# Optimization experiments

Measured on AMD Instinct MI355X. Metric: run time of the kernel, lower is better.

Reference implementation:

```python
import jax, jax.numpy as jnp
import numpy as np

E = 8        # num_experts
TOPK = 2     # num_experts_per_tok
D = 1024     # n_embd
H = 2816     # grok FFN hidden dim (multiple_of-rounded 2/3*4*D)
B, T = 4, 2048
COEFF = 0.01 # moe_aux_loss_coeff


def setup_inputs() -> dict:
    key = jax.random.key(0)
    ks = jax.random.split(key, 8)
    s = 0.02  # weight scale so activations stay well-conditioned
    return {
        "x": jax.random.normal(ks[0], (B, T, D), jnp.float32),
        "gate_w": jax.random.normal(ks[1], (D, E), jnp.float32) * s,
        "expert_gate": jax.random.normal(ks[2], (E, D, H), jnp.float32) * s,
        "expert_up": jax.random.normal(ks[3], (E, D, H), jnp.float32) * s,
        "expert_down": jax.random.normal(ks[4], (E, H, D), jnp.float32) * s,
        "shared_gate": jax.random.normal(ks[5], (D, H), jnp.float32) * s,
        "shared_up": jax.random.normal(ks[6], (D, H), jnp.float32) * s,
        "shared_down": jax.random.normal(ks[7], (H, D), jnp.float32) * s,
    }


def _grok_ffn(x, g, u, d):
    # down(gelu(gate(x)) * up(x)); torch F.gelu default = exact erf gelu
    return (jax.nn.gelu(x @ g, approximate=False) * (x @ u)) @ d


def reference(x, gate_w, expert_gate, expert_up, expert_down,
              shared_gate, shared_up, shared_down):
    Bb, Tt, Dd = x.shape
    N = Bb * Tt
    xf = x.reshape(N, Dd)

    # --- router ---
    logits = (xf @ gate_w).astype(jnp.float32)            # (N, E)
    top_logits, top_idx = jax.lax.top_k(logits, TOPK)     # (N, K)
    top_w = jax.nn.softmax(top_logits, axis=-1)           # (N, K)
    gates = jax.nn.softmax(logits, axis=-1)               # (N, E)
    f = jnp.mean(jax.nn.one_hot(top_idx[:, 0], E, dtype=jnp.float32), axis=0)
    P = gates.mean(axis=0)
    aux_loss = COEFF * E * jnp.sum(f * P)

    # dense combine weights (N, E): 0 for unassigned experts
    comb = jnp.zeros((N, E), xf.dtype).at[
        jnp.arange(N)[:, None], top_idx].add(top_w.astype(xf.dtype))

    # --- experts: loop over small fixed E, weight-masked dense FFN ---
    out = jnp.zeros_like(xf)
    for e in range(E):
        ye = _grok_ffn(xf, expert_gate[e], expert_up[e], expert_down[e])
        out = out + comb[:, e:e + 1] * ye

    out = out.reshape(Bb, Tt, Dd)
    out = out + _grok_ffn(xf, shared_gate, shared_up, shared_down).reshape(Bb, Tt, Dd)
    return out, aux_loss
```

## Files before the change

### kernel.cpp

```cpp
#include <hip/hip_runtime.h>
#include <hip/hip_bf16.h>

#define NTOK 8192
#define DIM  1024
#define HID  2816
#define ROWS_CAP 25600
#define TCAP 200

typedef __bf16 bf16x8 __attribute__((ext_vector_type(8)));
typedef float  f32x4  __attribute__((ext_vector_type(4)));

__device__ __forceinline__ unsigned short f2bf(float f) {
  unsigned int x = __float_as_uint(f);
  unsigned int r = (x + 0x7fffu + ((x >> 16) & 1u)) >> 16;
  return (unsigned short)r;
}
__device__ __forceinline__ float gelu_erf(float g) {
  return 0.5f * g * (1.0f + erff(g * 0.70710678118654752f));
}

__device__ __forceinline__ void gload16(const void* g, void* l) {
  __builtin_amdgcn_global_load_lds(
      (__attribute__((address_space(1))) void*)(g),
      (__attribute__((address_space(3))) void*)(l), 16, 0, 0);
}


__global__ __launch_bounds__(256) void k_cast_bf16(const float4* __restrict__ in,
                                                   ushort4* __restrict__ out, int n4) {
  int i = blockIdx.x * 256 + threadIdx.x;
  if (i >= n4) return;
  float4 v = in[i];
  out[i] = make_ushort4(f2bf(v.x), f2bf(v.y), f2bf(v.z), f2bf(v.w));
}

__global__ __launch_bounds__(256) void k_transpose_bf16(const float* __restrict__ in,
                                                        unsigned short* __restrict__ out,
                                                        int R, int C) {
  __shared__ float t[32][33];
  size_t base = (size_t)blockIdx.z * R * C;
  in += base; out += base;
  int c0 = blockIdx.x * 32, r0 = blockIdx.y * 32;
  int tx = threadIdx.x, ty = threadIdx.y;
  #pragma unroll
  for (int i = ty; i < 32; i += 8)
    t[i][tx] = in[(size_t)(r0 + i) * C + c0 + tx];
  __syncthreads();
  #pragma unroll
  for (int i = ty; i < 32; i += 8)
    out[(size_t)(c0 + i) * R + r0 + tx] = f2bf(t[tx][i]);
}


__global__ __launch_bounds__(256) void k_router(const float* __restrict__ x,
                                                const float* __restrict__ gw,
                                                int* __restrict__ top_idx,
                                                float* __restrict__ top_w,
                                                int* __restrict__ counts,
                                                float* __restrict__ f_cnt,
                                                float* __restrict__ P_sum) {
  __shared__ float s_p[8];
  __shared__ int   s_cnt[8];
  __shared__ int   s_f[8];
  int tid = threadIdx.x;
  if (tid < 8) { s_p[tid] = 0.f; s_cnt[tid] = 0; s_f[tid] = 0; }
  __syncthreads();

  int lane = tid & 63, wv = tid >> 6;
  float ploc[8] = {0,0,0,0,0,0,0,0};
  int   cloc[8] = {0,0,0,0,0,0,0,0};
  int   floc[8] = {0,0,0,0,0,0,0,0};

  for (int t = blockIdx.x * 4 + wv; t < NTOK; t += 1024) {
    const float* xr = x + (size_t)t * DIM;
    float acc[8] = {0.f,0.f,0.f,0.f,0.f,0.f,0.f,0.f};
    for (int d = lane; d < DIM; d += 64) {
      float xv = xr[d];
      const float* g = gw + d * 8;
      #pragma unroll
      for (int e = 0; e < 8; ++e) acc[e] += xv * g[e];
    }
    #pragma unroll
    for (int e = 0; e < 8; ++e) {
      #pragma unroll
      for (int off = 32; off > 0; off >>= 1)
        acc[e] += __shfl_xor(acc[e], off, 64);
    }
    if (lane == 0) {
      int i1 = 0; float l1 = acc[0];
      #pragma unroll
      for (int e = 1; e < 8; ++e) if (acc[e] > l1) { l1 = acc[e]; i1 = e; }
      int i2 = -1; float l2 = -3.0e38f;
      #pragma unroll
      for (int e = 0; e < 8; ++e) if (e != i1 && acc[e] > l2) { l2 = acc[e]; i2 = e; }
      float e2 = expf(l2 - l1);
      float inv12 = 1.0f / (1.0f + e2);
      top_idx[2 * t] = i1; top_idx[2 * t + 1] = i2;
      top_w[2 * t] = inv12; top_w[2 * t + 1] = e2 * inv12;
      float s = 0.f, p[8];
      #pragma unroll
      for (int e = 0; e < 8; ++e) { p[e] = expf(acc[e] - l1); s += p[e]; }
      float invs = 1.0f / s;
      #pragma unroll
      for (int e = 0; e < 8; ++e) {
        ploc[e] += p[e] * invs;
        cloc[e] += (e == i1) + (e == i2);
        floc[e] += (e == i1);
      }
    }
  }
  if (lane == 0) {
    #pragma unroll
    for (int e = 0; e < 8; ++e) {
      atomicAdd(&s_p[e], ploc[e]);
      atomicAdd(&s_cnt[e], cloc[e]);
      atomicAdd(&s_f[e], floc[e]);
    }
  }
  __syncthreads();
  if (tid < 8) {
    atomicAdd(&P_sum[tid], s_p[tid]);
    atomicAdd(&counts[tid], s_cnt[tid]);
    atomicAdd(&f_cnt[tid], (float)s_f[tid]);
  }
}


__global__ __launch_bounds__(256) void k_setup(const int* __restrict__ counts,
                                               int* __restrict__ cursors,
                                               int* __restrict__ tile_expert,
                                               int* __restrict__ tile_row0,
                                               int* __restrict__ perm,
                                               float* __restrict__ wrow) {
  int t = threadIdx.x;
  for (int r = t; r < ROWS_CAP; r += 256) {
    perm[r] = (r < NTOK) ? r : 0;
    wrow[r] = (r < NTOK) ? 1.0f : 0.0f;
  }
  if (t == 0) {
    int so[8], pe[8];
    int cur = NTOK;
    for (int e = 0; e < 8; ++e) {
      so[e] = cur;
      pe[e] = ((counts[e] + 127) >> 7) << 7;
      cur += pe[e];
    }
    for (int e = 0; e < 8; ++e) cursors[e] = so[e];
    for (int tile = 0; tile < TCAP; ++tile) {
      int r0 = tile << 7;
      int ex;
      if (tile < NTOK / 128) ex = 8;
      else if (r0 < cur) {
        ex = 0;
        for (int e = 0; e < 8; ++e) if (r0 >= so[e] && r0 < so[e] + pe[e]) ex = e;
      } else ex = -1;
      tile_expert[tile] = ex;
      tile_row0[tile] = r0;
    }
  }
}

__global__ __launch_bounds__(256) void k_scatter(const int* __restrict__ top_idx,
                                                 const float* __restrict__ top_w,
                                                 int* __restrict__ cursors,
                                                 int* __restrict__ perm,
                                                 float* __restrict__ wrow) {
  int i = blockIdx.x * 256 + threadIdx.x;
  if (i < NTOK * 2) {
    int e = top_idx[i];
    float w = top_w[i];
    int slot = atomicAdd(&cursors[e], 1);
    perm[slot] = i >> 1;
    wrow[slot] = w;
  }
}


__global__ __launch_bounds__(256) void k_stageA(const unsigned short* __restrict__ xb,
    const unsigned short* __restrict__ WgT, const unsigned short* __restrict__ WuT,
    const unsigned short* __restrict__ SgT, const unsigned short* __restrict__ SuT,
    const int* __restrict__ perm,
    const int* __restrict__ tile_expert, const int* __restrict__ tile_row0,
    unsigned short* __restrict__ h, int t0, int row_base) {
  int tile = t0 + blockIdx.y;
  int e = tile_expert[tile];
  if (e < 0) return;
  const unsigned short* Bg = (e < 8) ? WgT + (size_t)e * HID * DIM : SgT;
  const unsigned short* Bu = (e < 8) ? WuT + (size_t)e * HID * DIM : SuT;
  int rows0 = tile_row0[tile];
  int h0 = blockIdx.x * 64;

  __shared__ unsigned short As[128 * 64];
  __shared__ unsigned short Bgs[64 * 64];
  __shared__ unsigned short Bus[64 * 64];

  int tid = threadIdx.x, lane = tid & 63, wv = tid >> 6;
  int wr = wv >> 1, wc = wv & 1;
  int rlo = lane >> 3;
  int koff = (((lane & 7) ^ rlo) * 8);
  int rsw = (lane & 7) << 4;

  int prow[4];
  #pragma unroll
  for (int i = 0; i < 4; ++i) prow[i] = perm[rows0 + i * 32 + wv * 8 + rlo];
  int bn[2];
  #pragma unroll
  for (int i = 0; i < 2; ++i) bn[i] = h0 + i * 32 + wv * 8 + rlo;

  f32x4 accg[4][2] = {};
  f32x4 accu[4][2] = {};

  for (int kb = 0; kb < DIM / 64; ++kb) {
    int k0 = kb * 64;
    #pragma unroll
    for (int i = 0; i < 4; ++i)
      gload16(xb + (size_t)prow[i] * DIM + k0 + koff, (char*)As + (i * 32 + wv * 8) * 128);
    #pragma unroll
    for (int i = 0; i < 2; ++i) {
      gload16(Bg + (size_t)bn[i] * DIM + k0 + koff, (char*)Bgs + (i * 32 + wv * 8) * 128);
      gload16(Bu + (size_t)bn[i] * DIM + k0 + koff, (char*)Bus + (i * 32 + wv * 8) * 128);
    }
    __syncthreads();
    #pragma unroll
    for (int kk = 0; kk < 2; ++kk) {
      int kbyte = (kk * 64 + (lane >> 4) * 16) ^ rsw;
      bf16x8 a[4], bg[2], bu[2];
      #pragma unroll
      for (int mi = 0; mi < 4; ++mi)
        a[mi] = *(const bf16x8*)((const char*)As + (wr * 64 + mi * 16 + (lane & 15)) * 128 + kbyte);
      #pragma unroll
      for (int ni = 0; ni < 2; ++ni) {
        bg[ni] = *(const bf16x8*)((const char*)Bgs + (wc * 32 + ni * 16 + (lane & 15)) * 128 + kbyte);
        bu[ni] = *(const bf16x8*)((const char*)Bus + (wc * 32 + ni * 16 + (lane & 15)) * 128 + kbyte);
      }
      #pragma unroll
      for (int mi = 0; mi < 4; ++mi) {
        #pragma unroll
        for (int ni = 0; ni < 2; ++ni) {
          accg[mi][ni] = __builtin_amdgcn_mfma_f32_16x16x32_bf16(a[mi], bg[ni], accg[mi][ni], 0, 0, 0);
          accu[mi][ni] = __builtin_amdgcn_mfma_f32_16x16x32_bf16(a[mi], bu[ni], accu[mi][ni], 0, 0, 0);
        }
      }
    }
    __syncthreads();
  }
  #pragma unroll
  for (int mi = 0; mi < 4; ++mi) {
    #pragma unroll
    for (int ni = 0; ni < 2; ++ni) {
      #pragma unroll
      for (int j = 0; j < 4; ++j) {
        int rg = rows0 - row_base + wr * 64 + mi * 16 + (lane >> 4) * 4 + j;
        int cg = h0 + wc * 32 + ni * 16 + (lane & 15);
        float g = accg[mi][ni][j];
        float u = accu[mi][ni][j];
        h[(size_t)rg * HID + cg] = f2bf(gelu_erf(g) * u);
      }
    }
  }
}


template <bool STORE>
__global__ __launch_bounds__(256) void k_stageB(const unsigned short* __restrict__ h,
    const unsigned short* __restrict__ WdT, const unsigned short* __restrict__ SdT,
    const int* __restrict__ perm, const float* __restrict__ wrow,
    const int* __restrict__ tile_expert, const int* __restrict__ tile_row0,
    float* __restrict__ out, int t0, int row_base) {
  int tile = t0 + blockIdx.y;
  int e = tile_expert[tile];
  if (e < 0) return;
  const unsigned short* Bd = (e < 8) ? WdT + (size_t)e * DIM * HID : SdT;
  int rows0 = tile_row0[tile];
  int n0 = blockIdx.x * 128;

  __shared__ unsigned short As[128 * 64];
  __shared__ unsigned short Bs[128 * 64];

  int tid = threadIdx.x, lane = tid & 63, wv = tid >> 6;
  int wr = wv >> 1, wc = wv & 1;
  int rlo = lane >> 3;
  int koff = (((lane & 7) ^ rlo) * 8);
  int rsw = (lane & 7) << 4;

  f32x4 acc[4][4] = {};

  for (int kb = 0; kb < HID / 64; ++kb) {
    int k0 = kb * 64;
    #pragma unroll
    for (int i = 0; i < 4; ++i) {
      int rb = i * 32 + wv * 8;
      int r = rb + rlo;
      gload16(h + (size_t)(rows0 - row_base + r) * HID + k0 + koff, (char*)As + rb * 128);
      gload16(Bd + (size_t)(n0 + r) * HID + k0 + koff, (char*)Bs + rb * 128);
    }
    __syncthreads();
    #pragma unroll
    for (int kk = 0; kk < 2; ++kk) {
      int kbyte = (kk * 64 + (lane >> 4) * 16) ^ rsw;
      bf16x8 a[4], b[4];
      #pragma unroll
      for (int mi = 0; mi < 4; ++mi)
        a[mi] = *(const bf16x8*)((const char*)As + (wr * 64 + mi * 16 + (lane & 15)) * 128 + kbyte);
      #pragma unroll
      for (int ni = 0; ni < 4; ++ni)
        b[ni] = *(const bf16x8*)((const char*)Bs + (wc * 64 + ni * 16 + (lane & 15)) * 128 + kbyte);
      #pragma unroll
      for (int mi = 0; mi < 4; ++mi) {
        #pragma unroll
        for (int ni = 0; ni < 4; ++ni)
          acc[mi][ni] = __builtin_amdgcn_mfma_f32_16x16x32_bf16(a[mi], b[ni], acc[mi][ni], 0, 0, 0);
      }
    }
    __syncthreads();
  }
  #pragma unroll
  for (int mi = 0; mi < 4; ++mi) {
    #pragma unroll
    for (int j = 0; j < 4; ++j) {
      int rl = wr * 64 + mi * 16 + (lane >> 4) * 4 + j;
      int token = perm[rows0 + rl];
      float w = wrow[rows0 + rl];
      #pragma unroll
      for (int ni = 0; ni < 4; ++ni) {
        int col = n0 + wc * 64 + ni * 16 + (lane & 15);
        if (STORE) out[(size_t)token * DIM + col] = w * acc[mi][ni][j];
        else atomicAdd(&out[(size_t)token * DIM + col], w * acc[mi][ni][j]);
      }
    }
  }
}


__global__ void k_aux(const float* __restrict__ f_cnt, const float* __restrict__ P_sum,
                      float* __restrict__ aux_out) {
  if (threadIdx.x == 0 && blockIdx.x == 0) {
    float a = 0.f;
    #pragma unroll
    for (int e = 0; e < 8; ++e) a += f_cnt[e] * P_sum[e];
    a *= 0.01f * 8.f / ((float)NTOK * (float)NTOK);
    aux_out[0] = a;
  }
}


extern "C" void kernel_launch(void* const* d_in, const int* in_sizes, int n_in,
                              void* d_out, int out_size, void* d_ws, size_t ws_size,
                              hipStream_t stream) {
  const float* x  = (const float*)d_in[0];
  const float* gw = (const float*)d_in[1];
  const float* eg = (const float*)d_in[2];
  const float* eu = (const float*)d_in[3];
  const float* ed = (const float*)d_in[4];
  const float* sg = (const float*)d_in[5];
  const float* su = (const float*)d_in[6];
  const float* sd = (const float*)d_in[7];
  float* out = (float*)d_out;

  char* ws = (char*)d_ws;
  size_t off = 0;
  auto take = [&](size_t sz) { size_t o = off; off += (sz + 255) & ~(size_t)255; return o; };
  const size_t OFF_XB   = take((size_t)NTOK * DIM * 2);
  const size_t OFF_WGT  = take((size_t)8 * HID * DIM * 2);
  const size_t OFF_WUT  = take((size_t)8 * HID * DIM * 2);
  const size_t OFF_WDT  = take((size_t)8 * HID * DIM * 2);
  const size_t OFF_SGT  = take((size_t)HID * DIM * 2);
  const size_t OFF_SUT  = take((size_t)HID * DIM * 2);
  const size_t OFF_SDT  = take((size_t)HID * DIM * 2);
  const size_t OFF_TI   = take((size_t)NTOK * 2 * 4);
  const size_t OFF_TW   = take((size_t)NTOK * 2 * 4);
  const size_t OFF_PERM = take((size_t)ROWS_CAP * 4);
  const size_t OFF_WROW = take((size_t)ROWS_CAP * 4);
  const size_t OFF_STATS= take(256);
  const size_t OFF_CURS = take(256);
  const size_t OFF_TE   = take(TCAP * 4);
  const size_t OFF_TR   = take(TCAP * 4);
  const size_t OFF_H    = off;

  const size_t TILE_H_BYTES = (size_t)128 * HID * 2;
  size_t avail = (ws_size > OFF_H) ? (ws_size - OFF_H) : 0;
  int G = (int)((avail / TILE_H_BYTES < (size_t)TCAP) ? (avail / TILE_H_BYTES) : (size_t)TCAP);
  if (G < 1) return;

  unsigned short* xb  = (unsigned short*)(ws + OFF_XB);
  unsigned short* WgT = (unsigned short*)(ws + OFF_WGT);
  unsigned short* WuT = (unsigned short*)(ws + OFF_WUT);
  unsigned short* WdT = (unsigned short*)(ws + OFF_WDT);
  unsigned short* SgT = (unsigned short*)(ws + OFF_SGT);
  unsigned short* SuT = (unsigned short*)(ws + OFF_SUT);
  unsigned short* SdT = (unsigned short*)(ws + OFF_SDT);
  int* top_idx        = (int*)(ws + OFF_TI);
  float* top_w        = (float*)(ws + OFF_TW);
  int* perm           = (int*)(ws + OFF_PERM);
  float* wrow         = (float*)(ws + OFF_WROW);
  int* counts         = (int*)(ws + OFF_STATS);
  float* f_cnt        = (float*)(ws + OFF_STATS + 32);
  float* P_sum        = (float*)(ws + OFF_STATS + 64);
  int* cursors        = (int*)(ws + OFF_CURS);
  int* tile_expert    = (int*)(ws + OFF_TE);
  int* tile_row0      = (int*)(ws + OFF_TR);
  unsigned short* hbuf = (unsigned short*)(ws + OFF_H);

  hipMemsetAsync(ws + OFF_STATS, 0, 256, stream);

  k_cast_bf16<<<NTOK * DIM / 4 / 256, 256, 0, stream>>>((const float4*)x, (ushort4*)xb, NTOK * DIM / 4);
  k_transpose_bf16<<<dim3(HID / 32, DIM / 32, 8), dim3(32, 8), 0, stream>>>(eg, WgT, DIM, HID);
  k_transpose_bf16<<<dim3(HID / 32, DIM / 32, 8), dim3(32, 8), 0, stream>>>(eu, WuT, DIM, HID);
  k_transpose_bf16<<<dim3(DIM / 32, HID / 32, 8), dim3(32, 8), 0, stream>>>(ed, WdT, HID, DIM);
  k_transpose_bf16<<<dim3(HID / 32, DIM / 32, 1), dim3(32, 8), 0, stream>>>(sg, SgT, DIM, HID);
  k_transpose_bf16<<<dim3(HID / 32, DIM / 32, 1), dim3(32, 8), 0, stream>>>(su, SuT, DIM, HID);
  k_transpose_bf16<<<dim3(DIM / 32, HID / 32, 1), dim3(32, 8), 0, stream>>>(sd, SdT, HID, DIM);

  k_router<<<256, 256, 0, stream>>>(x, gw, top_idx, top_w, counts, f_cnt, P_sum);
  k_setup<<<1, 256, 0, stream>>>(counts, cursors, tile_expert, tile_row0, perm, wrow);
  k_scatter<<<NTOK * 2 / 256, 256, 0, stream>>>(top_idx, top_w, cursors, perm, wrow);

  for (int t0 = 0; t0 < TCAP; t0 += G) {
    int nt = (TCAP - t0 < G) ? (TCAP - t0) : G;
    int row_base = t0 * 128;
    k_stageA<<<dim3(HID / 64, nt), 256, 0, stream>>>(xb, WgT, WuT, SgT, SuT, perm,
                                                     tile_expert, tile_row0, hbuf, t0, row_base);
    int ns = 0;
    if (t0 < 64) { ns = 64 - t0; if (ns > nt) ns = nt; }
    int ne = nt - ns;
    if (ns > 0)
      k_stageB<true><<<dim3(DIM / 128, ns), 256, 0, stream>>>(hbuf, WdT, SdT, perm, wrow,
                                                              tile_expert, tile_row0, out, t0, row_base);
    if (ne > 0)
      k_stageB<false><<<dim3(DIM / 128, ne), 256, 0, stream>>>(hbuf, WdT, SdT, perm, wrow,
                                                               tile_expert, tile_row0, out, t0 + ns, row_base);
  }

  k_aux<<<1, 64, 0, stream>>>(f_cnt, P_sum, out + (size_t)NTOK * DIM);
}
```

Measured before the change: 1.065 ms.

## Double-buffer LDS tiles in MoE GEMM stages to overlap loads with MFMA

Both expert GEMM kernels (gate/up stage and down stage) now use two LDS buffers. The next K-slice is prefetched with global_load_lds while MFMAs run on the current slice, and there is one barrier per iteration instead of two. Row pointers are precomputed and wave priority is raised around the MFMA block. LDS usage doubles per block, which may reduce occupancy.

Result: no change. 1.072 ms (+0.7%).

```diff
diff --git a/kernel.cpp b/kernel.cpp
--- a/kernel.cpp
+++ b/kernel.cpp
@@ -23,6 +23,12 @@
   __builtin_amdgcn_global_load_lds(
       (__attribute__((address_space(1))) void*)(g),
       (__attribute__((address_space(3))) void*)(l), 16, 0, 0);
+}
+
+__device__ __forceinline__ void pipe_barrier() {
+  asm volatile("s_waitcnt vmcnt(0)" ::: "memory");
+  __builtin_amdgcn_s_barrier();
+  __builtin_amdgcn_sched_barrier(0);
 }
 
 
@@ -190,9 +196,9 @@
   int rows0 = tile_row0[tile];
   int h0 = blockIdx.x * 64;
 
-  __shared__ unsigned short As[128 * 64];
-  __shared__ unsigned short Bgs[64 * 64];
-  __shared__ unsigned short Bus[64 * 64];
+  __shared__ unsigned short As[2][128 * 64];
+  __shared__ unsigned short Bgs[2][64 * 64];
+  __shared__ unsigned short Bus[2][64 * 64];
 
   int tid = threadIdx.x, lane = tid & 63, wv = tid >> 6;
   int wr = wv >> 1, wc = wv & 1;
@@ -200,38 +206,51 @@
   int koff = (((lane & 7) ^ rlo) * 8);
   int rsw = (lane & 7) << 4;
 
-  int prow[4];
-  #pragma unroll
-  for (int i = 0; i < 4; ++i) prow[i] = perm[rows0 + i * 32 + wv * 8 + rlo];
-  int bn[2];
-  #pragma unroll
-  for (int i = 0; i < 2; ++i) bn[i] = h0 + i * 32 + wv * 8 + rlo;
+  const unsigned short* ap[4];
+  #pragma unroll
+  for (int i = 0; i < 4; ++i)
+    ap[i] = xb + (size_t)perm[rows0 + i * 32 + wv * 8 + rlo] * DIM + koff;
+  const unsigned short* bgp[2];
+  const unsigned short* bup[2];
+  #pragma unroll
+  for (int i = 0; i < 2; ++i) {
+    int bn = h0 + i * 32 + wv * 8 + rlo;
+    bgp[i] = Bg + (size_t)bn * DIM + koff;
+    bup[i] = Bu + (size_t)bn * DIM + koff;
+  }
 
   f32x4 accg[4][2] = {};
   f32x4 accu[4][2] = {};
 
+  auto stage = [&](int b, int k0) {
+    #pragma unroll
+    for (int i = 0; i < 4; ++i)
+      gload16(ap[i] + k0, (char*)As[b] + (i * 32 + wv * 8) * 128);
+    #pragma unroll
+    for (int i = 0; i < 2; ++i) {
+      gload16(bgp[i] + k0, (char*)Bgs[b] + (i * 32 + wv * 8) * 128);
+      gload16(bup[i] + k0, (char*)Bus[b] + (i * 32 + wv * 8) * 128);
+    }
+  };
+
+  stage(0, 0);
+  pipe_barrier();
+  int cur = 0;
+
   for (int kb = 0; kb < DIM / 64; ++kb) {
-    int k0 = kb * 64;
-    #pragma unroll
-    for (int i = 0; i < 4; ++i)
-      gload16(xb + (size_t)prow[i] * DIM + k0 + koff, (char*)As + (i * 32 + wv * 8) * 128);
-    #pragma unroll
-    for (int i = 0; i < 2; ++i) {
-      gload16(Bg + (size_t)bn[i] * DIM + k0 + koff, (char*)Bgs + (i * 32 + wv * 8) * 128);
-      gload16(Bu + (size_t)bn[i] * DIM + k0 + koff, (char*)Bus + (i * 32 + wv * 8) * 128);
-    }
-    __syncthreads();
+    if (kb < DIM / 64 - 1) stage(cur ^ 1, (kb + 1) * 64);
+    __builtin_amdgcn_s_setprio(1);
     #pragma unroll
     for (int kk = 0; kk < 2; ++kk) {
       int kbyte = (kk * 64 + (lane >> 4) * 16) ^ rsw;
       bf16x8 a[4], bg[2], bu[2];
       #pragma unroll
       for (int mi = 0; mi < 4; ++mi)
-        a[mi] = *(const bf16x8*)((const char*)As + (wr * 64 + mi * 16 + (lane & 15)) * 128 + kbyte);
+        a[mi] = *(const bf16x8*)((const char*)As[cur] + (wr * 64 + mi * 16 + (lane & 15)) * 128 + kbyte);
       #pragma unroll
       for (int ni = 0; ni < 2; ++ni) {
-        bg[ni] = *(const bf16x8*)((const char*)Bgs + (wc * 32 + ni * 16 + (lane & 15)) * 128 + kbyte);
-        bu[ni] = *(const bf16x8*)((const char*)Bus + (wc * 32 + ni * 16 + (lane & 15)) * 128 + kbyte);
+        bg[ni] = *(const bf16x8*)((const char*)Bgs[cur] + (wc * 32 + ni * 16 + (lane & 15)) * 128 + kbyte);
+        bu[ni] = *(const bf16x8*)((const char*)Bus[cur] + (wc * 32 + ni * 16 + (lane & 15)) * 128 + kbyte);
       }
       #pragma unroll
       for (int mi = 0; mi < 4; ++mi) {
@@ -242,8 +261,11 @@
         }
       }
     }
-    __syncthreads();
-  }
+    __builtin_amdgcn_s_setprio(0);
+    pipe_barrier();
+    cur ^= 1;
+  }
+
   #pragma unroll
   for (int mi = 0; mi < 4; ++mi) {
     #pragma unroll
@@ -274,8 +296,8 @@
   int rows0 = tile_row0[tile];
   int n0 = blockIdx.x * 128;
 
-  __shared__ unsigned short As[128 * 64];
-  __shared__ unsigned short Bs[128 * 64];
+  __shared__ unsigned short As[2][128 * 64];
+  __shared__ unsigned short Bs[2][128 * 64];
 
   int tid = threadIdx.x, lane = tid & 63, wv = tid >> 6;
   int wr = wv >> 1, wc = wv & 1;
@@ -283,28 +305,43 @@
   int koff = (((lane & 7) ^ rlo) * 8);
   int rsw = (lane & 7) << 4;
 
+  const unsigned short* apt[4];
+  const unsigned short* bpt[4];
+  #pragma unroll
+  for (int i = 0; i < 4; ++i) {
+    int r = i * 32 + wv * 8 + rlo;
+    apt[i] = h + (size_t)(rows0 - row_base + r) * HID + koff;
+    bpt[i] = Bd + (size_t)(n0 + r) * HID + koff;
+  }
+
   f32x4 acc[4][4] = {};
 
-  for (int kb = 0; kb < HID / 64; ++kb) {
-    int k0 = kb * 64;
+  auto stage = [&](int b, int k0) {
     #pragma unroll
     for (int i = 0; i < 4; ++i) {
       int rb = i * 32 + wv * 8;
-      int r = rb + rlo;
-      gload16(h + (size_t)(rows0 - row_base + r) * HID + k0 + koff, (char*)As + rb * 128);
-      gload16(Bd + (size_t)(n0 + r) * HID + k0 + koff, (char*)Bs + rb * 128);
-    }
-    __syncthreads();
+      gload16(apt[i] + k0, (char*)As[b] + rb * 128);
+      gload16(bpt[i] + k0, (char*)Bs[b] + rb * 128);
+    }
+  };
+
+  stage(0, 0);
+  pipe_barrier();
+  int cur = 0;
+
+  for (int kb = 0; kb < HID / 64; ++kb) {
+    if (kb < HID / 64 - 1) stage(cur ^ 1, (kb + 1) * 64);
+    __builtin_amdgcn_s_setprio(1);
     #pragma unroll
     for (int kk = 0; kk < 2; ++kk) {
       int kbyte = (kk * 64 + (lane >> 4) * 16) ^ rsw;
       bf16x8 a[4], b[4];
       #pragma unroll
       for (int mi = 0; mi < 4; ++mi)
-        a[mi] = *(const bf16x8*)((const char*)As + (wr * 64 + mi * 16 + (lane & 15)) * 128 + kbyte);
+        a[mi] = *(const bf16x8*)((const char*)As[cur] + (wr * 64 + mi * 16 + (lane & 15)) * 128 + kbyte);
       #pragma unroll
       for (int ni = 0; ni < 4; ++ni)
-        b[ni] = *(const bf16x8*)((const char*)Bs + (wc * 64 + ni * 16 + (lane & 15)) * 128 + kbyte);
+        b[ni] = *(const bf16x8*)((const char*)Bs[cur] + (wc * 64 + ni * 16 + (lane & 15)) * 128 + kbyte);
       #pragma unroll
       for (int mi = 0; mi < 4; ++mi) {
         #pragma unroll
@@ -312,8 +349,11 @@
           acc[mi][ni] = __builtin_amdgcn_mfma_f32_16x16x32_bf16(a[mi], b[ni], acc[mi][ni], 0, 0, 0);
       }
     }
-    __syncthreads();
-  }
+    __builtin_amdgcn_s_setprio(0);
+    pipe_barrier();
+    cur ^= 1;
+  }
+
   #pragma unroll
   for (int mi = 0; mi < 4; ++mi) {
     #pragma unroll
```
